# Kernel optimization log

Hardware: AMD Instinct MI355X
Metric: run time of the kernel (lower is better)

The kernel has to match this reference:

```python
import jax, jax.numpy as jnp
import numpy as np

EPS = 1e-5
C = 512


def conv1x1(x, w, b):
    # 1x1 conv == per-pixel linear: x [B,C,H,W], w [O,C], b [O]
    return jnp.einsum('bchw,oc->bohw', x, w) + b[None, :, None, None]


def mean_variance_norm(feat):
    # per (batch, channel) normalization over spatial dims, unbiased var + eps
    b, c, h, w = feat.shape
    flat = feat.reshape(b, c, h * w)
    mean = flat.mean(axis=2)[:, :, None, None]
    std = jnp.sqrt(jnp.var(flat, axis=2, ddof=1) + EPS)[:, :, None, None]
    return (feat - mean) / std


def setup_inputs() -> dict:
    key = jax.random.key(0)
    ks = jax.random.split(key, 10)
    sc = 1.0 / np.sqrt(C)
    inp = {
        'content': jax.random.normal(ks[0], (2, C, 64, 64), jnp.float32),
        'style': jax.random.normal(ks[1], (2, C, 64, 64), jnp.float32),
        'f_w': jax.random.normal(ks[2], (C, C), jnp.float32) * sc,
        'f_b': jnp.zeros((C,), jnp.float32),
        'g_w': jax.random.normal(ks[3], (C, C), jnp.float32) * sc,
        'g_b': jnp.zeros((C,), jnp.float32),
        'h_w': jax.random.normal(ks[4], (C, C), jnp.float32) * sc,
        'h_b': jnp.zeros((C,), jnp.float32),
        'out_w': jax.random.normal(ks[5], (C, C), jnp.float32) * sc,
        'out_b': jnp.zeros((C,), jnp.float32),
    }
    return inp


def reference(content, style, f_w, f_b, g_w, g_b, h_w, h_b, out_w, out_b):
    b, c, h, w = content.shape
    Fq = conv1x1(content, f_w, f_b).reshape(b, c, h * w).transpose(0, 2, 1)  # [b,Nc,C]
    Gk = conv1x1(style, g_w, g_b).reshape(b, c, -1)                           # [b,C,Ns]
    Hv = conv1x1(style, h_w, h_b).reshape(b, c, -1).transpose(0, 2, 1)        # [b,Ns,C]

    S = jax.nn.softmax(jnp.einsum('bnc,bcs->bns', Fq, Gk), axis=-1)           # [b,Nc,Ns]
    mean = jnp.einsum('bns,bsc->bnc', S, Hv)                                   # E[x]
    second = jnp.einsum('bns,bsc->bnc', S, Hv * Hv)                            # E[x^2]
    std = jnp.sqrt(jnp.maximum(second - mean * mean, 0.0))

    mean = mean.reshape(b, h, w, c).transpose(0, 3, 1, 2)
    std = std.reshape(b, h, w, c).transpose(0, 3, 1, 2)

    O = std * mean_variance_norm(content) + mean
    O = conv1x1(O, out_w, out_b)
    return O + content
```

## Files before the change

### kernel.cpp

```cpp
#include <hip/hip_runtime.h>
#include <math.h>

#define NS 4096
#define CH 512
#define EPSV 1e-5f

typedef __attribute__((ext_vector_type(8))) _Float16 f16x8;
typedef __attribute__((ext_vector_type(4))) float f32x4;
typedef unsigned short u16;

__device__ __forceinline__ u16 f2h(float x) {
    _Float16 h = (_Float16)x;
    return __builtin_bit_cast(unsigned short, h);
}
__device__ __forceinline__ float h2f(u16 b) {
    return (float)__builtin_bit_cast(_Float16, b);
}

__device__ __forceinline__ void gload16(const void* g, void* l) {
    __builtin_amdgcn_global_load_lds((const __attribute__((address_space(1))) unsigned*)g,
                                     (__attribute__((address_space(3))) unsigned*)l, 16, 0, 0);
}

struct ZTab {
    long aoff[6];
    long boff[6];
    long ooff[6];
    int  mode[6];
    int  np[6];
    const float* bias[6];
};

template<int NPZ>
__device__ __forceinline__ void kloop(
    const u16* __restrict__ pAhi, const u16* __restrict__ pAlo,
    const u16* __restrict__ pBhi, const u16* __restrict__ pBlo,
    u16* smem, int smemStride,
    int Mw, int Nw, int K, int m0, int n0,
    int wid, int lane, int lk, int lm, int wm, int wn,
    f32x4 (&acc)[4][4])
{
    auto stage = [&](int buf, int ks) {
        const int kp0 = ks << 2;
        #pragma unroll
        for (int i = 0; i < 2 * NPZ; ++i) {
            const int q = i * 4 + wid;
            const int b = q >> 3;
            const int p = (q & 7) >> 1;
            const int w = ((q & 1) << 6) + lane;
            const u16* src;
            if (b == 0)      src = pAhi + ((size_t)(kp0 + p) * Mw + m0 + w) * 8;
            else if (b == 1) src = pBhi + ((size_t)(kp0 + p) * Nw + n0 + w) * 8;
            else if (b == 2) src = pAlo + ((size_t)(kp0 + p) * Mw + m0 + w) * 8;
            else             src = pBlo + ((size_t)(kp0 + p) * Nw + n0 + w) * 8;
            gload16(src, &smem[(size_t)buf * smemStride + (size_t)(((b * 4 + p) * 128) + w) * 8]);
        }
    };

    const int nK = K >> 5;
    stage(0, 0);
    __syncthreads();
    int cur = 0;
    for (int ks = 0; ks < nK; ++ks) {
        if (ks + 1 < nK) stage(cur ^ 1, ks + 1);
        const u16* sm = smem + (size_t)cur * smemStride;
        f16x8 ah[4], bh[4], al[4], bl[4];
        #pragma unroll
        for (int f = 0; f < 4; ++f) {
            ah[f] = *(const f16x8*)&sm[((0 * 4 + lk) * 128 + wm * 64 + f * 16 + lm) * 8];
            bh[f] = *(const f16x8*)&sm[((1 * 4 + lk) * 128 + wn * 64 + f * 16 + lm) * 8];
            if (NPZ >= 3)
                al[f] = *(const f16x8*)&sm[((2 * 4 + lk) * 128 + wm * 64 + f * 16 + lm) * 8];
            if (NPZ == 4)
                bl[f] = *(const f16x8*)&sm[((3 * 4 + lk) * 128 + wn * 64 + f * 16 + lm) * 8];
        }
        #pragma unroll
        for (int i = 0; i < 4; ++i)
            #pragma unroll
            for (int j = 0; j < 4; ++j) {
                acc[i][j] = __builtin_amdgcn_mfma_f32_16x16x32_f16(ah[i], bh[j], acc[i][j], 0, 0, 0);
                if (NPZ >= 3)
                    acc[i][j] = __builtin_amdgcn_mfma_f32_16x16x32_f16(al[i], bh[j], acc[i][j], 0, 0, 0);
                if (NPZ == 4)
                    acc[i][j] = __builtin_amdgcn_mfma_f32_16x16x32_f16(ah[i], bl[j], acc[i][j], 0, 0, 0);
            }
        __syncthreads();
        cur ^= 1;
    }
}

template<int NP, bool RESID, bool COLST>
__global__ __launch_bounds__(256, (NP == 2 ? 4 : (NP == 3 ? 3 : 2))) void gemm_split(
    const u16* __restrict__ Ahi, const u16* __restrict__ Alo,
    const u16* __restrict__ Bhi, const u16* __restrict__ Blo,
    const float* __restrict__ resid,
    float* __restrict__ outF, u16* __restrict__ outH,
    float* __restrict__ pmg, float* __restrict__ psg,
    int Mw, int Nw, int K, ZTab tab)
{
    __shared__ u16 smem[2][NP * 4 * 128 * 8];
    const int t = threadIdx.x;
    const int lane = t & 63;
    const int wid = t >> 6;
    const int wm = wid >> 1, wn = wid & 1;
    const int lk = lane >> 4, lm = lane & 15;
    const int m0 = blockIdx.y * 128, n0 = blockIdx.x * 128;
    const int z = blockIdx.z;
    const int npz = tab.np[z];
    const u16* pAhi = Ahi + tab.aoff[z];
    const u16* pAlo = Alo + tab.aoff[z];
    const u16* pBhi = Bhi + tab.boff[z];
    const u16* pBlo = (NP == 4) ? (Blo + tab.boff[z]) : nullptr;

    f32x4 acc[4][4] = {};
    const int smemStride = NP * 4 * 128 * 8;

    if constexpr (NP == 2) {
        kloop<2>(pAhi, pAlo, pBhi, pBlo, &smem[0][0], smemStride,
                 Mw, Nw, K, m0, n0, wid, lane, lk, lm, wm, wn, acc);
    } else if constexpr (NP == 3) {
        if (npz == 2)
            kloop<2>(pAhi, pAlo, pBhi, pBlo, &smem[0][0], smemStride,
                     Mw, Nw, K, m0, n0, wid, lane, lk, lm, wm, wn, acc);
        else
            kloop<3>(pAhi, pAlo, pBhi, pBlo, &smem[0][0], smemStride,
                     Mw, Nw, K, m0, n0, wid, lane, lk, lm, wm, wn, acc);
    } else {
        kloop<4>(pAhi, pAlo, pBhi, pBlo, &smem[0][0], smemStride,
                 Mw, Nw, K, m0, n0, wid, lane, lk, lm, wm, wn, acc);
    }

    const float* bp = tab.bias[z];
    if (COLST) {
        float mxj[4];
        #pragma unroll
        for (int j = 0; j < 4; ++j) {
            float mx = -3.0e38f;
            #pragma unroll
            for (int i = 0; i < 4; ++i)
                #pragma unroll
                for (int r = 0; r < 4; ++r)
                    mx = fmaxf(mx, acc[i][j][r]);
            mx = fmaxf(mx, __shfl_xor(mx, 16));
            mx = fmaxf(mx, __shfl_xor(mx, 32));
            mxj[j] = mx;
            float sum = 0.f;
            #pragma unroll
            for (int i = 0; i < 4; ++i)
                #pragma unroll
                for (int r = 0; r < 4; ++r)
                    sum += __expf(acc[i][j][r] - mx);
            sum += __shfl_xor(sum, 16);
            sum += __shfl_xor(sum, 32);
            if (lk == 0) {
                const int n = n0 + wn * 64 + j * 16 + lm;
                const int grp = (m0 >> 6) + wm;
                pmg[((size_t)z * 64 + grp) * NS + n] = mx;
                psg[((size_t)z * 64 + grp) * NS + n] = sum;
            }
        }
        u16* ph = outH + tab.ooff[z];
        #pragma unroll
        for (int i = 0; i < 4; ++i) {
            const long rg = (long)((m0 + wm * 64) >> 3) + i * 2 + (lk >> 1);
            const int sub = (lk & 1) * 4;
            #pragma unroll
            for (int j = 0; j < 4; ++j) {
                const int n = n0 + wn * 64 + j * 16 + lm;
                const long idx = (rg * Nw + n) * 8 + sub;
                u16 h[4];
                #pragma unroll
                for (int r = 0; r < 4; ++r)
                    h[r] = f2h(acc[i][j][r] - mxj[j]);
                *(ushort4*)&ph[idx] = make_ushort4(h[0], h[1], h[2], h[3]);
            }
        }
    } else if (tab.mode[z] == 0) {
        float* pout = outF + tab.ooff[z];
        #pragma unroll
        for (int i = 0; i < 4; ++i) {
            #pragma unroll
            for (int r = 0; r < 4; ++r) {
                const int m = m0 + wm * 64 + i * 16 + lk * 4 + r;
                const float bv = bp ? bp[m] : 0.f;
                const size_t ro = (size_t)m * Nw + n0 + wn * 64 + lm;
                #pragma unroll
                for (int j = 0; j < 4; ++j) {
                    float v = acc[i][j][r] + bv;
                    if (RESID) v += resid[tab.ooff[z] + ro + j * 16];
                    pout[ro + j * 16] = v;
                }
            }
        }
    } else {
        u16* ph = outH + tab.ooff[z];
        #pragma unroll
        for (int i = 0; i < 4; ++i) {
            float bv[4];
            #pragma unroll
            for (int r = 0; r < 4; ++r) {
                const int m = m0 + wm * 64 + i * 16 + lk * 4 + r;
                bv[r] = bp ? bp[m] : 0.f;
            }
            const long rg = (long)((m0 + wm * 64) >> 3) + i * 2 + (lk >> 1);
            const int sub = (lk & 1) * 4;
            #pragma unroll
            for (int j = 0; j < 4; ++j) {
                const int n = n0 + wn * 64 + j * 16 + lm;
                const long idx = (rg * Nw + n) * 8 + sub;
                u16 h[4];
                #pragma unroll
                for (int r = 0; r < 4; ++r)
                    h[r] = f2h(acc[i][j][r] + bv[r]);
                *(ushort4*)&ph[idx] = make_ushort4(h[0], h[1], h[2], h[3]);
            }
        }
    }
}

__global__ __launch_bounds__(256) void packB_k(const float* __restrict__ X,
    u16* __restrict__ Hi, int Nw, long xB, long pB)
{
    const int n = blockIdx.x * 256 + threadIdx.x;
    const int p = blockIdx.y;
    const int z = blockIdx.z;
    const float* Xp = X + (size_t)z * xB + ((size_t)p * 8) * Nw + n;
    u16 hi[8];
    #pragma unroll
    for (int j = 0; j < 8; ++j)
        hi[j] = f2h(Xp[(size_t)j * Nw]);
    const size_t o = (size_t)z * pB + ((size_t)p * Nw + n) * 8;
    *(uint4*)&Hi[o] = *(const uint4*)hi;
}

__global__ __launch_bounds__(256) void pack_P(const u16* __restrict__ S16,
    const float* __restrict__ pm, const float* __restrict__ mxv,
    const float* __restrict__ invv, u16* __restrict__ Pp)
{
    const int n = blockIdx.x * 256 + threadIdx.x;
    const int rg = blockIdx.y;
    const int z = blockIdx.z;
    const long NSNS = (long)NS * NS;
    const int g = rg >> 3;
    const float shift = pm[((size_t)z * 64 + g) * NS + n] - mxv[(size_t)z * NS + n];
    const float inv = invv[(size_t)z * NS + n];
    const size_t idx = (size_t)z * NSNS + ((size_t)rg * NS + n) * 8;
    uint4 sv = *(const uint4*)&S16[idx];
    const u16* s = (const u16*)&sv;
    u16 p[8];
    #pragma unroll
    for (int j = 0; j < 8; ++j)
        p[j] = f2h(__expf(h2f(s[j]) + shift) * inv);
    *(uint4*)&Pp[idx] = *(const uint4*)p;
}

__global__ __launch_bounds__(256) void packA_T(const float* __restrict__ W,
    u16* __restrict__ Hi, u16* __restrict__ Lo, int Kdim)
{
    __shared__ float tile[64][65];
    const int t = threadIdx.x;
    const int k0 = blockIdx.x * 64, m0 = blockIdx.y * 64;
    const int kk = t & 63, mb = t >> 6;
    #pragma unroll
    for (int it = 0; it < 16; ++it) {
        int mm = mb + it * 4;
        tile[mm][kk] = W[(size_t)(m0 + mm) * Kdim + k0 + kk];
    }
    __syncthreads();
    #pragma unroll
    for (int cc = 0; cc < 2; ++cc) {
        int c = t + cc * 256;
        int kp = c >> 6, m = c & 63;
        u16 hi[8], lo[8];
        #pragma unroll
        for (int j = 0; j < 8; ++j) {
            float v = tile[m][kp * 8 + j];
            u16 h = f2h(v);
            hi[j] = h;
            lo[j] = f2h(v - h2f(h));
        }
        size_t o = ((size_t)(k0 / 8 + kp) * CH + m0 + m) * 8;
        *(uint4*)&Hi[o] = *(const uint4*)hi;
        *(uint4*)&Lo[o] = *(const uint4*)lo;
    }
}

__global__ __launch_bounds__(256) void pack_hvT(const float* __restrict__ Hv,
    u16* __restrict__ H1h, u16* __restrict__ H2h, u16* __restrict__ H2l)
{
    __shared__ float tile[64][65];
    const int t = threadIdx.x;
    const int s0 = blockIdx.x * 64, c0 = blockIdx.y * 64;
    const int z = blockIdx.z;
    const float* src = Hv + (size_t)z * CH * NS;
    const int ss = t & 63, cb = t >> 6;
    #pragma unroll
    for (int it = 0; it < 16; ++it) {
        int cc = cb + it * 4;
        tile[cc][ss] = src[(size_t)(c0 + cc) * NS + s0 + ss];
    }
    __syncthreads();
    const size_t zb = (size_t)z * NS * CH;
    #pragma unroll
    for (int cc2 = 0; cc2 < 2; ++cc2) {
        int c = t + cc2 * 256;
        int sp = c >> 6, cm = c & 63;
        u16 h1[8], h2[8], l2[8];
        #pragma unroll
        for (int j = 0; j < 8; ++j) {
            float v = tile[cm][sp * 8 + j];
            u16 a = f2h(v);
            h1[j] = a;
            float q = h2f(a);
            float q2 = q * q;
            u16 b = f2h(q2);
            h2[j] = b;
            l2[j] = f2h(q2 - h2f(b));
        }
        size_t o = zb + ((size_t)(s0 / 8 + sp) * CH + c0 + cm) * 8;
        *(uint4*)&H1h[o] = *(const uint4*)h1;
        *(uint4*)&H2h[o] = *(const uint4*)h2;
        *(uint4*)&H2l[o] = *(const uint4*)l2;
    }
}

__global__ __launch_bounds__(256) void colstats_comb64(const float* __restrict__ pm,
    const float* __restrict__ ps, float* __restrict__ mx, float* __restrict__ inv)
{
    const int n = blockIdx.x * 256 + threadIdx.x;
    const int z = blockIdx.y;
    float m = -3.0e38f, s = 0.f;
    #pragma unroll 8
    for (int g = 0; g < 64; ++g) {
        float gm = pm[((size_t)z * 64 + g) * NS + n], gs = ps[((size_t)z * 64 + g) * NS + n];
        float nm = fmaxf(m, gm);
        s = s * __expf(m - nm) + gs * __expf(gm - nm);
        m = nm;
    }
    mx[(size_t)z * NS + n] = m;
    inv[(size_t)z * NS + n] = 1.f / s;
}

__global__ __launch_bounds__(256) void content_stats(const float* __restrict__ content,
                                                     float* __restrict__ cmean,
                                                     float* __restrict__ cinv)
{
    const int bc = blockIdx.x;
    const float4* p = (const float4*)(content + (size_t)bc * NS);
    const int t = threadIdx.x;
    float s = 0.f, s2 = 0.f;
    #pragma unroll
    for (int j = 0; j < 4; ++j) {
        float4 v = p[t + j * 256];
        s  += (v.x + v.y) + (v.z + v.w);
        s2 += (v.x * v.x + v.y * v.y) + (v.z * v.z + v.w * v.w);
    }
    #pragma unroll
    for (int off = 32; off >= 1; off >>= 1) {
        s  += __shfl_xor(s, off);
        s2 += __shfl_xor(s2, off);
    }
    __shared__ float r1[4], r2[4];
    const int wid = t >> 6;
    if ((t & 63) == 0) { r1[wid] = s; r2[wid] = s2; }
    __syncthreads();
    if (t == 0) {
        s  = (r1[0] + r1[1]) + (r1[2] + r1[3]);
        s2 = (r2[0] + r2[1]) + (r2[2] + r2[3]);
        const float mean = s * (1.0f / 4096.f);
        const float var = (s2 - 4096.f * mean * mean) * (1.0f / 4095.f);
        cmean[bc] = mean;
        cinv[bc] = rsqrtf(fmaxf(var, 0.f) + EPSV);
    }
}

__global__ __launch_bounds__(256) void compute_O_pack(
    const float* __restrict__ Mean, const float* __restrict__ Sec,
    const float* __restrict__ content,
    const float* __restrict__ cmean, const float* __restrict__ cinv,
    u16* __restrict__ Oh)
{
    const int n  = blockIdx.x * 256 + threadIdx.x;
    const int cg = blockIdx.y;
    const int b  = blockIdx.z;
    const size_t KN = (size_t)CH * NS;
    u16 h[8];
    #pragma unroll
    for (int j = 0; j < 8; ++j) {
        const int c = cg * 8 + j;
        const size_t po = (size_t)b * KN + (size_t)c * NS + n;
        const float mn = Mean[po];
        const float sc = Sec[po];
        const float ct = content[po];
        const int bc = b * CH + c;
        const float o = sqrtf(fmaxf(sc - mn * mn, 0.f)) * ((ct - cmean[bc]) * cinv[bc]) + mn;
        h[j] = f2h(o);
    }
    const size_t off = (size_t)b * KN + ((size_t)cg * NS + n) * 8;
    *(uint4*)&Oh[off] = *(const uint4*)h;
}

extern "C" void kernel_launch(void* const* d_in, const int* in_sizes, int n_in,
                              void* d_out, int out_size, void* d_ws, size_t ws_size,
                              hipStream_t stream)
{
    const float* content = (const float*)d_in[0];
    const float* style   = (const float*)d_in[1];
    const float* f_w   = (const float*)d_in[2];
    const float* f_b   = (const float*)d_in[3];
    const float* g_w   = (const float*)d_in[4];
    const float* g_b   = (const float*)d_in[5];
    const float* h_w   = (const float*)d_in[6];
    const float* h_b   = (const float*)d_in[7];
    const float* out_w = (const float*)d_in[8];
    const float* out_b = (const float*)d_in[9];
    float* out = (float*)d_out;

    char* ws = (char*)d_ws;
    size_t off = 0;
    auto alloc = [&](size_t bytes) -> void* {
        void* p = ws + off;
        off = (off + bytes + 255) & ~(size_t)255;
        return p;
    };

    const size_t KN   = (size_t)CH * NS;
    const size_t CHCH = (size_t)CH * CH;
    const long   NSNS = (long)NS * NS;

    u16 *Wh[4], *Wl[4];
    for (int w = 0; w < 4; ++w) { Wh[w] = (u16*)alloc(CHCH * 2); Wl[w] = (u16*)alloc(CHCH * 2); }

    u16* R2 = (u16*)alloc(8 * KN * 2);
    u16* Xc_hi = R2;
    u16* Xs_hi = R2 + 2 * KN;
    u16* HvT_hi  = R2;
    u16* Hv2T_hi = R2 + 2 * KN;
    u16* Hv2T_lo = R2 + 4 * KN;

    u16* Fqp_hi = (u16*)alloc(2 * KN * 2);
    u16* Gkp_hi = (u16*)alloc(2 * KN * 2);
    u16* Op_hi  = Gkp_hi;

    u16* Pp = (u16*)alloc(2 * (size_t)NS * NS * 2);

    char* R5 = (char*)alloc(2 * (size_t)NS * NS * 2);
    float* Hv32 = (float*)(R5 + 4 * KN * 4);
    u16*   S16  = (u16*)R5;

    float* Mean32 = (float*)alloc(2 * KN * 4);
    float* Sec32  = (float*)alloc(2 * KN * 4);

    float* pm    = (float*)alloc(2 * 64 * NS * 4);
    float* ps    = (float*)alloc(2 * 64 * NS * 4);
    float* mxv   = (float*)alloc(2 * NS * 4);
    float* invv  = (float*)alloc(2 * NS * 4);
    float* cmean = (float*)alloc(1024 * 4);
    float* cinv  = (float*)alloc(1024 * 4);
    (void)ws_size; (void)in_sizes; (void)n_in; (void)out_size;

    packA_T<<<dim3(8, 8), 256, 0, stream>>>(f_w,   Wh[0], Wl[0], CH);
    packA_T<<<dim3(8, 8), 256, 0, stream>>>(g_w,   Wh[1], Wl[1], CH);
    packA_T<<<dim3(8, 8), 256, 0, stream>>>(h_w,   Wh[2], Wl[2], CH);
    packA_T<<<dim3(8, 8), 256, 0, stream>>>(out_w, Wh[3], Wl[3], CH);
    packB_k<<<dim3(16, 64, 2), 256, 0, stream>>>(content, Xc_hi, NS, (long)KN, (long)KN);
    packB_k<<<dim3(16, 64, 2), 256, 0, stream>>>(style,   Xs_hi, NS, (long)KN, (long)KN);
    content_stats<<<1024, 256, 0, stream>>>(content, cmean, cinv);

    {
        ZTab tb = {};
        const float* bs[3] = { f_b, g_b, h_b };
        for (int z = 0; z < 6; ++z) {
            const int w = z >> 1, b = z & 1;
            tb.aoff[z] = (long)(2 * w) * CHCH;
            tb.boff[z] = (w == 0 ? 0 : (long)(2 * KN)) + (long)b * KN;
            tb.mode[z] = (w < 2) ? 1 : 0;
            tb.np[z]   = 3;
            tb.ooff[z] = (w < 2) ? ((long)w * 2 * KN + (long)b * KN)
                                 : ((long)4 * KN + (long)b * KN);
            tb.bias[z] = bs[w];
        }
        gemm_split<3, false, false><<<dim3(32, 4, 6), 256, 0, stream>>>(
            Wh[0], Wh[0] + CHCH, Xc_hi, nullptr, nullptr,
            (float*)R5, Fqp_hi, nullptr, nullptr, CH, NS, CH, tb);
    }

    pack_hvT<<<dim3(64, 8, 2), 256, 0, stream>>>(Hv32, HvT_hi, Hv2T_hi, Hv2T_lo);

    {
        ZTab tq = {};
        for (int z = 0; z < 2; ++z) {
            tq.aoff[z] = (long)z * KN;
            tq.boff[z] = (long)z * KN;
            tq.ooff[z] = (long)z * NSNS;
            tq.np[z]   = 2;
        }
        gemm_split<2, false, true><<<dim3(32, 32, 2), 256, 0, stream>>>(
            Gkp_hi, nullptr, Fqp_hi, nullptr, nullptr,
            nullptr, S16, pm, ps, NS, NS, CH, tq);
    }
    colstats_comb64<<<dim3(16, 2), 256, 0, stream>>>(pm, ps, mxv, invv);
    pack_P<<<dim3(16, 512, 2), 256, 0, stream>>>(S16, pm, mxv, invv, Pp);

    {
        ZTab tp = {};
        for (int z = 0; z < 4; ++z) {
            const int sec = (z >> 1), b = z & 1;
            tp.aoff[z] = (long)sec * 2 * KN + (long)b * KN;
            tp.boff[z] = (long)b * NSNS;
            tp.ooff[z] = (long)sec * 2 * KN + (long)b * KN;
            tp.np[z]   = sec ? 3 : 2;
        }
        gemm_split<3, false, false><<<dim3(32, 4, 4), 256, 0, stream>>>(
            R2, R2 + 2 * KN, Pp, nullptr, nullptr,
            Mean32, nullptr, nullptr, nullptr, CH, NS, NS, tp);
    }

    compute_O_pack<<<dim3(16, 64, 2), 256, 0, stream>>>(
        Mean32, Sec32, content, cmean, cinv, Op_hi);

    {
        ZTab tf = {};
        for (int z = 0; z < 2; ++z) {
            tf.ooff[z] = (long)z * KN;
            tf.boff[z] = (long)z * KN;
            tf.np[z]   = 3;
            tf.bias[z] = out_b;
        }
        gemm_split<3, true, false><<<dim3(32, 4, 2), 256, 0, stream>>>(
            Wh[3], Wh[3] + CHCH, Op_hi, nullptr, content,
            out, nullptr, nullptr, nullptr, CH, NS, CH, tf);
    }
}
```

Baseline: 262.7 us.

## Fuse softmax exp into QK GEMM, apply per-group scale in PV GEMM, drop weight lo-split

The QK GEMM epilogue now combines the two warp-row max/sum partials in shared memory and writes exp(s - blockmax) in fp16 directly, halving the partial-stat groups. The separate pack_P pass over the full NSxNS matrix is removed. The PV GEMM instead accumulates each 128-row K group into a temporary and rescales it by a per-column factor from a small scale_c kernel. The hi/lo split of the weights for the 1x1 convs is also dropped (np 3 to 2), which cuts MFMA work but lowers precision of those projections.

```diff
diff --git a/kernel.cpp b/kernel.cpp
--- a/kernel.cpp
+++ b/kernel.cpp
@@ -26,18 +26,20 @@
     long aoff[6];
     long boff[6];
     long ooff[6];
+    long coff[6];
     int  mode[6];
     int  np[6];
     const float* bias[6];
 };
 
-template<int NPZ>
+template<int NPZ, bool GS>
 __device__ __forceinline__ void kloop(
     const u16* __restrict__ pAhi, const u16* __restrict__ pAlo,
-    const u16* __restrict__ pBhi, const u16* __restrict__ pBlo,
+    const u16* __restrict__ pBhi,
     u16* smem, int smemStride,
     int Mw, int Nw, int K, int m0, int n0,
     int wid, int lane, int lk, int lm, int wm, int wn,
+    const float* __restrict__ cbase, const int* nidx,
     f32x4 (&acc)[4][4])
 {
     auto stage = [&](int buf, int ks) {
@@ -51,51 +53,85 @@
             const u16* src;
             if (b == 0)      src = pAhi + ((size_t)(kp0 + p) * Mw + m0 + w) * 8;
             else if (b == 1) src = pBhi + ((size_t)(kp0 + p) * Nw + n0 + w) * 8;
-            else if (b == 2) src = pAlo + ((size_t)(kp0 + p) * Mw + m0 + w) * 8;
-            else             src = pBlo + ((size_t)(kp0 + p) * Nw + n0 + w) * 8;
+            else             src = pAlo + ((size_t)(kp0 + p) * Mw + m0 + w) * 8;
             gload16(src, &smem[(size_t)buf * smemStride + (size_t)(((b * 4 + p) * 128) + w) * 8]);
+        }
+    };
+    auto frags = [&](int buf, f16x8 (&ah)[4], f16x8 (&bh)[4], f16x8 (&al)[4]) {
+        const u16* sm = smem + (size_t)buf * smemStride;
+        #pragma unroll
+        for (int f = 0; f < 4; ++f) {
+            ah[f] = *(const f16x8*)&sm[((0 * 4 + lk) * 128 + wm * 64 + f * 16 + lm) * 8];
+            bh[f] = *(const f16x8*)&sm[((1 * 4 + lk) * 128 + wn * 64 + f * 16 + lm) * 8];
+            if (NPZ == 3)
+                al[f] = *(const f16x8*)&sm[((2 * 4 + lk) * 128 + wm * 64 + f * 16 + lm) * 8];
         }
     };
 
     const int nK = K >> 5;
     stage(0, 0);
     __syncthreads();
-    int cur = 0;
-    for (int ks = 0; ks < nK; ++ks) {
-        if (ks + 1 < nK) stage(cur ^ 1, ks + 1);
-        const u16* sm = smem + (size_t)cur * smemStride;
-        f16x8 ah[4], bh[4], al[4], bl[4];
-        #pragma unroll
-        for (int f = 0; f < 4; ++f) {
-            ah[f] = *(const f16x8*)&sm[((0 * 4 + lk) * 128 + wm * 64 + f * 16 + lm) * 8];
-            bh[f] = *(const f16x8*)&sm[((1 * 4 + lk) * 128 + wn * 64 + f * 16 + lm) * 8];
-            if (NPZ >= 3)
-                al[f] = *(const f16x8*)&sm[((2 * 4 + lk) * 128 + wm * 64 + f * 16 + lm) * 8];
-            if (NPZ == 4)
-                bl[f] = *(const f16x8*)&sm[((3 * 4 + lk) * 128 + wn * 64 + f * 16 + lm) * 8];
-        }
-        #pragma unroll
-        for (int i = 0; i < 4; ++i)
-            #pragma unroll
-            for (int j = 0; j < 4; ++j) {
-                acc[i][j] = __builtin_amdgcn_mfma_f32_16x16x32_f16(ah[i], bh[j], acc[i][j], 0, 0, 0);
-                if (NPZ >= 3)
-                    acc[i][j] = __builtin_amdgcn_mfma_f32_16x16x32_f16(al[i], bh[j], acc[i][j], 0, 0, 0);
-                if (NPZ == 4)
-                    acc[i][j] = __builtin_amdgcn_mfma_f32_16x16x32_f16(ah[i], bl[j], acc[i][j], 0, 0, 0);
-            }
-        __syncthreads();
-        cur ^= 1;
-    }
-}
-
-template<int NP, bool RESID, bool COLST>
-__global__ __launch_bounds__(256, (NP == 2 ? 4 : (NP == 3 ? 3 : 2))) void gemm_split(
+    if constexpr (GS) {
+        const f32x4 zf = {0.f, 0.f, 0.f, 0.f};
+        const int nG = nK >> 2;
+        for (int g = 0; g < nG; ++g) {
+            float cg[4];
+            #pragma unroll
+            for (int j = 0; j < 4; ++j)
+                cg[j] = cbase[(size_t)g * NS + nidx[j]];
+            f32x4 part[4][4];
+            #pragma unroll
+            for (int kk = 0; kk < 4; ++kk) {
+                const int ks = g * 4 + kk;
+                if (ks + 1 < nK) stage((kk & 1) ^ 1, ks + 1);
+                f16x8 ah[4], bh[4], al[4];
+                frags(kk & 1, ah, bh, al);
+                #pragma unroll
+                for (int i = 0; i < 4; ++i)
+                    #pragma unroll
+                    for (int j = 0; j < 4; ++j) {
+                        part[i][j] = __builtin_amdgcn_mfma_f32_16x16x32_f16(
+                            ah[i], bh[j], (kk == 0 ? zf : part[i][j]), 0, 0, 0);
+                        if (NPZ == 3)
+                            part[i][j] = __builtin_amdgcn_mfma_f32_16x16x32_f16(
+                                al[i], bh[j], part[i][j], 0, 0, 0);
+                    }
+                __syncthreads();
+            }
+            #pragma unroll
+            for (int i = 0; i < 4; ++i)
+                #pragma unroll
+                for (int j = 0; j < 4; ++j)
+                    acc[i][j] += part[i][j] * cg[j];
+        }
+    } else {
+        int cur = 0;
+        for (int ks = 0; ks < nK; ++ks) {
+            if (ks + 1 < nK) stage(cur ^ 1, ks + 1);
+            f16x8 ah[4], bh[4], al[4];
+            frags(cur, ah, bh, al);
+            #pragma unroll
+            for (int i = 0; i < 4; ++i)
+                #pragma unroll
+                for (int j = 0; j < 4; ++j) {
+                    acc[i][j] = __builtin_amdgcn_mfma_f32_16x16x32_f16(ah[i], bh[j], acc[i][j], 0, 0, 0);
+                    if (NPZ == 3)
+                        acc[i][j] = __builtin_amdgcn_mfma_f32_16x16x32_f16(al[i], bh[j], acc[i][j], 0, 0, 0);
+                }
+            __syncthreads();
+            cur ^= 1;
+        }
+    }
+}
+
+template<int NP, bool RESID, bool COLST, bool GS>
+__global__ __launch_bounds__(256, (NP == 2 ? 4 : 3)) void gemm_split(
     const u16* __restrict__ Ahi, const u16* __restrict__ Alo,
-    const u16* __restrict__ Bhi, const u16* __restrict__ Blo,
+    const u16* __restrict__ Bhi,
     const float* __restrict__ resid,
     float* __restrict__ outF, u16* __restrict__ outH,
     float* __restrict__ pmg, float* __restrict__ psg,
+    const float* __restrict__ cb,
     int Mw, int Nw, int K, ZTab tab)
 {
     __shared__ u16 smem[2][NP * 4 * 128 * 8];
@@ -110,29 +146,31 @@
     const u16* pAhi = Ahi + tab.aoff[z];
     const u16* pAlo = Alo + tab.aoff[z];
     const u16* pBhi = Bhi + tab.boff[z];
-    const u16* pBlo = (NP == 4) ? (Blo + tab.boff[z]) : nullptr;
+    const float* cbase = GS ? (cb + tab.coff[z]) : nullptr;
+    int nidx[4];
+    #pragma unroll
+    for (int j = 0; j < 4; ++j) nidx[j] = n0 + wn * 64 + j * 16 + lm;
 
     f32x4 acc[4][4] = {};
     const int smemStride = NP * 4 * 128 * 8;
 
     if constexpr (NP == 2) {
-        kloop<2>(pAhi, pAlo, pBhi, pBlo, &smem[0][0], smemStride,
-                 Mw, Nw, K, m0, n0, wid, lane, lk, lm, wm, wn, acc);
-    } else if constexpr (NP == 3) {
+        kloop<2, GS>(pAhi, pAlo, pBhi, &smem[0][0], smemStride,
+                     Mw, Nw, K, m0, n0, wid, lane, lk, lm, wm, wn, cbase, nidx, acc);
+    } else {
         if (npz == 2)
-            kloop<2>(pAhi, pAlo, pBhi, pBlo, &smem[0][0], smemStride,
-                     Mw, Nw, K, m0, n0, wid, lane, lk, lm, wm, wn, acc);
+            kloop<2, GS>(pAhi, pAlo, pBhi, &smem[0][0], smemStride,
+                         Mw, Nw, K, m0, n0, wid, lane, lk, lm, wm, wn, cbase, nidx, acc);
         else
-            kloop<3>(pAhi, pAlo, pBhi, pBlo, &smem[0][0], smemStride,
-                     Mw, Nw, K, m0, n0, wid, lane, lk, lm, wm, wn, acc);
-    } else {
-        kloop<4>(pAhi, pAlo, pBhi, pBlo, &smem[0][0], smemStride,
-                 Mw, Nw, K, m0, n0, wid, lane, lk, lm, wm, wn, acc);
+            kloop<3, GS>(pAhi, pAlo, pBhi, &smem[0][0], smemStride,
+                         Mw, Nw, K, m0, n0, wid, lane, lk, lm, wm, wn, cbase, nidx, acc);
     }
 
     const float* bp = tab.bias[z];
     if (COLST) {
-        float mxj[4];
+        float* smx = (float*)&smem[0][0];
+        float* ssm = smx + 256;
+        float mxw[4], smw[4];
         #pragma unroll
         for (int j = 0; j < 4; ++j) {
             float mx = -3.0e38f;
@@ -143,7 +181,6 @@
                     mx = fmaxf(mx, acc[i][j][r]);
             mx = fmaxf(mx, __shfl_xor(mx, 16));
             mx = fmaxf(mx, __shfl_xor(mx, 32));
-            mxj[j] = mx;
             float sum = 0.f;
             #pragma unroll
             for (int i = 0; i < 4; ++i)
@@ -152,11 +189,27 @@
                     sum += __expf(acc[i][j][r] - mx);
             sum += __shfl_xor(sum, 16);
             sum += __shfl_xor(sum, 32);
+            mxw[j] = mx; smw[j] = sum;
             if (lk == 0) {
-                const int n = n0 + wn * 64 + j * 16 + lm;
-                const int grp = (m0 >> 6) + wm;
-                pmg[((size_t)z * 64 + grp) * NS + n] = mx;
-                psg[((size_t)z * 64 + grp) * NS + n] = sum;
+                const int nloc = wn * 64 + j * 16 + lm;
+                smx[wm * 128 + nloc] = mx;
+                ssm[wm * 128 + nloc] = sum;
+            }
+        }
+        __syncthreads();
+        float mxc[4];
+        #pragma unroll
+        for (int j = 0; j < 4; ++j) {
+            const int nloc = wn * 64 + j * 16 + lm;
+            const float m0v = smx[nloc], m1v = smx[128 + nloc];
+            const float mc = fmaxf(m0v, m1v);
+            mxc[j] = mc;
+            if (wm == 0 && lk == 0) {
+                const float sc = ssm[nloc] * __expf(m0v - mc) + ssm[128 + nloc] * __expf(m1v - mc);
+                const int n = n0 + nloc;
+                const size_t gi = ((size_t)z * 32 + (m0 >> 7)) * NS + n;
+                pmg[gi] = mc;
+                psg[gi] = sc;
             }
         }
         u16* ph = outH + tab.ooff[z];
@@ -171,7 +224,7 @@
                 u16 h[4];
                 #pragma unroll
                 for (int r = 0; r < 4; ++r)
-                    h[r] = f2h(acc[i][j][r] - mxj[j]);
+                    h[r] = f2h(__expf(acc[i][j][r] - mxc[j]));
                 *(ushort4*)&ph[idx] = make_ushort4(h[0], h[1], h[2], h[3]);
             }
         }
@@ -233,29 +286,8 @@
     *(uint4*)&Hi[o] = *(const uint4*)hi;
 }
 
-__global__ __launch_bounds__(256) void pack_P(const u16* __restrict__ S16,
-    const float* __restrict__ pm, const float* __restrict__ mxv,
-    const float* __restrict__ invv, u16* __restrict__ Pp)
-{
-    const int n = blockIdx.x * 256 + threadIdx.x;
-    const int rg = blockIdx.y;
-    const int z = blockIdx.z;
-    const long NSNS = (long)NS * NS;
-    const int g = rg >> 3;
-    const float shift = pm[((size_t)z * 64 + g) * NS + n] - mxv[(size_t)z * NS + n];
-    const float inv = invv[(size_t)z * NS + n];
-    const size_t idx = (size_t)z * NSNS + ((size_t)rg * NS + n) * 8;
-    uint4 sv = *(const uint4*)&S16[idx];
-    const u16* s = (const u16*)&sv;
-    u16 p[8];
-    #pragma unroll
-    for (int j = 0; j < 8; ++j)
-        p[j] = f2h(__expf(h2f(s[j]) + shift) * inv);
-    *(uint4*)&Pp[idx] = *(const uint4*)p;
-}
-
 __global__ __launch_bounds__(256) void packA_T(const float* __restrict__ W,
-    u16* __restrict__ Hi, u16* __restrict__ Lo, int Kdim)
+    u16* __restrict__ Hi, int Kdim)
 {
     __shared__ float tile[64][65];
     const int t = threadIdx.x;
@@ -271,17 +303,12 @@
     for (int cc = 0; cc < 2; ++cc) {
         int c = t + cc * 256;
         int kp = c >> 6, m = c & 63;
-        u16 hi[8], lo[8];
-        #pragma unroll
-        for (int j = 0; j < 8; ++j) {
-            float v = tile[m][kp * 8 + j];
-            u16 h = f2h(v);
-            hi[j] = h;
-            lo[j] = f2h(v - h2f(h));
-        }
+        u16 hi[8];
+        #pragma unroll
+        for (int j = 0; j < 8; ++j)
+            hi[j] = f2h(tile[m][kp * 8 + j]);
         size_t o = ((size_t)(k0 / 8 + kp) * CH + m0 + m) * 8;
         *(uint4*)&Hi[o] = *(const uint4*)hi;
-        *(uint4*)&Lo[o] = *(const uint4*)lo;
     }
 }
 
@@ -324,21 +351,32 @@
     }
 }
 
-__global__ __launch_bounds__(256) void colstats_comb64(const float* __restrict__ pm,
+__global__ __launch_bounds__(256) void colstats_comb32(const float* __restrict__ pm,
     const float* __restrict__ ps, float* __restrict__ mx, float* __restrict__ inv)
 {
     const int n = blockIdx.x * 256 + threadIdx.x;
     const int z = blockIdx.y;
     float m = -3.0e38f, s = 0.f;
     #pragma unroll 8
-    for (int g = 0; g < 64; ++g) {
-        float gm = pm[((size_t)z * 64 + g) * NS + n], gs = ps[((size_t)z * 64 + g) * NS + n];
+    for (int g = 0; g < 32; ++g) {
+        float gm = pm[((size_t)z * 32 + g) * NS + n], gs = ps[((size_t)z * 32 + g) * NS + n];
         float nm = fmaxf(m, gm);
         s = s * __expf(m - nm) + gs * __expf(gm - nm);
         m = nm;
     }
     mx[(size_t)z * NS + n] = m;
     inv[(size_t)z * NS + n] = 1.f / s;
+}
+
+__global__ __launch_bounds__(256) void scale_c(const float* __restrict__ pm,
+    const float* __restrict__ mxv, const float* __restrict__ invv,
+    float* __restrict__ c)
+{
+    const int n = blockIdx.x * 256 + threadIdx.x;
+    const int g = blockIdx.y;
+    const int z = blockIdx.z;
+    const size_t gi = ((size_t)z * 32 + g) * NS + n;
+    c[gi] = __expf(pm[gi] - mxv[(size_t)z * NS + n]) * invv[(size_t)z * NS + n];
 }
 
 __global__ __launch_bounds__(256) void content_stats(const float* __restrict__ content,
@@ -428,10 +466,10 @@
     const size_t CHCH = (size_t)CH * CH;
     const long   NSNS = (long)NS * NS;
 
-    u16 *Wh[4], *Wl[4];
-    for (int w = 0; w < 4; ++w) { Wh[w] = (u16*)alloc(CHCH * 2); Wl[w] = (u16*)alloc(CHCH * 2); }
-
-    u16* R2 = (u16*)alloc(8 * KN * 2);
+    u16* Wh0 = (u16*)alloc(4 * CHCH * 2);
+    u16* Whv[4] = { Wh0, Wh0 + CHCH, Wh0 + 2 * CHCH, Wh0 + 3 * CHCH };
+
+    u16* R2 = (u16*)alloc(6 * KN * 2);
     u16* Xc_hi = R2;
     u16* Xs_hi = R2 + 2 * KN;
     u16* HvT_hi  = R2;
@@ -442,27 +480,26 @@
     u16* Gkp_hi = (u16*)alloc(2 * KN * 2);
     u16* Op_hi  = Gkp_hi;
 
-    u16* Pp = (u16*)alloc(2 * (size_t)NS * NS * 2);
-
     char* R5 = (char*)alloc(2 * (size_t)NS * NS * 2);
     float* Hv32 = (float*)(R5 + 4 * KN * 4);
-    u16*   S16  = (u16*)R5;
+    u16*   E16  = (u16*)R5;
 
     float* Mean32 = (float*)alloc(2 * KN * 4);
     float* Sec32  = (float*)alloc(2 * KN * 4);
 
-    float* pm    = (float*)alloc(2 * 64 * NS * 4);
-    float* ps    = (float*)alloc(2 * 64 * NS * 4);
+    float* pm    = (float*)alloc(2 * 32 * NS * 4);
+    float* ps    = (float*)alloc(2 * 32 * NS * 4);
     float* mxv   = (float*)alloc(2 * NS * 4);
     float* invv  = (float*)alloc(2 * NS * 4);
+    float* ctab  = (float*)alloc(2 * 32 * NS * 4);
     float* cmean = (float*)alloc(1024 * 4);
     float* cinv  = (float*)alloc(1024 * 4);
     (void)ws_size; (void)in_sizes; (void)n_in; (void)out_size;
 
-    packA_T<<<dim3(8, 8), 256, 0, stream>>>(f_w,   Wh[0], Wl[0], CH);
-    packA_T<<<dim3(8, 8), 256, 0, stream>>>(g_w,   Wh[1], Wl[1], CH);
-    packA_T<<<dim3(8, 8), 256, 0, stream>>>(h_w,   Wh[2], Wl[2], CH);
-    packA_T<<<dim3(8, 8), 256, 0, stream>>>(out_w, Wh[3], Wl[3], CH);
+    packA_T<<<dim3(8, 8), 256, 0, stream>>>(f_w,   Whv[0], CH);
+    packA_T<<<dim3(8, 8), 256, 0, stream>>>(g_w,   Whv[1], CH);
+    packA_T<<<dim3(8, 8), 256, 0, stream>>>(h_w,   Whv[2], CH);
+    packA_T<<<dim3(8, 8), 256, 0, stream>>>(out_w, Whv[3], CH);
     packB_k<<<dim3(16, 64, 2), 256, 0, stream>>>(content, Xc_hi, NS, (long)KN, (long)KN);
     packB_k<<<dim3(16, 64, 2), 256, 0, stream>>>(style,   Xs_hi, NS, (long)KN, (long)KN);
     content_stats<<<1024, 256, 0, stream>>>(content, cmean, cinv);
@@ -472,17 +509,17 @@
         const float* bs[3] = { f_b, g_b, h_b };
         for (int z = 0; z < 6; ++z) {
             const int w = z >> 1, b = z & 1;
-            tb.aoff[z] = (long)(2 * w) * CHCH;
+            tb.aoff[z] = (long)w * CHCH;
             tb.boff[z] = (w == 0 ? 0 : (long)(2 * KN)) + (long)b * KN;
             tb.mode[z] = (w < 2) ? 1 : 0;
-            tb.np[z]   = 3;
+            tb.np[z]   = 2;
             tb.ooff[z] = (w < 2) ? ((long)w * 2 * KN + (long)b * KN)
                                  : ((long)4 * KN + (long)b * KN);
             tb.bias[z] = bs[w];
         }
-        gemm_split<3, false, false><<<dim3(32, 4, 6), 256, 0, stream>>>(
-            Wh[0], Wh[0] + CHCH, Xc_hi, nullptr, nullptr,
-            (float*)R5, Fqp_hi, nullptr, nullptr, CH, NS, CH, tb);
+        gemm_split<2, false, false, false><<<dim3(32, 4, 6), 256, 0, stream>>>(
+            Wh0, nullptr, Xc_hi, nullptr,
+            (float*)R5, Fqp_hi, nullptr, nullptr, nullptr, CH, NS, CH, tb);
     }
 
     pack_hvT<<<dim3(64, 8, 2), 256, 0, stream>>>(Hv32, HvT_hi, Hv2T_hi, Hv2T_lo);
@@ -495,12 +532,12 @@
             tq.ooff[z] = (long)z * NSNS;
             tq.np[z]   = 2;
         }
-        gemm_split<2, false, true><<<dim3(32, 32, 2), 256, 0, stream>>>(
-            Gkp_hi, nullptr, Fqp_hi, nullptr, nullptr,
-            nullptr, S16, pm, ps, NS, NS, CH, tq);
-    }
-    colstats_comb64<<<dim3(16, 2), 256, 0, stream>>>(pm, ps, mxv, invv);
-    pack_P<<<dim3(16, 512, 2), 256, 0, stream>>>(S16, pm, mxv, invv, Pp);
+        gemm_split<2, false, true, false><<<dim3(32, 32, 2), 256, 0, stream>>>(
+            Gkp_hi, nullptr, Fqp_hi, nullptr,
+            nullptr, E16, pm, ps, nullptr, NS, NS, CH, tq);
+    }
+    colstats_comb32<<<dim3(16, 2), 256, 0, stream>>>(pm, ps, mxv, invv);
+    scale_c<<<dim3(16, 32, 2), 256, 0, stream>>>(pm, mxv, invv, ctab);
 
     {
         ZTab tp = {};
@@ -509,11 +546,12 @@
             tp.aoff[z] = (long)sec * 2 * KN + (long)b * KN;
             tp.boff[z] = (long)b * NSNS;
             tp.ooff[z] = (long)sec * 2 * KN + (long)b * KN;
+            tp.coff[z] = (long)b * 32 * NS;
             tp.np[z]   = sec ? 3 : 2;
         }
-        gemm_split<3, false, false><<<dim3(32, 4, 4), 256, 0, stream>>>(
-            R2, R2 + 2 * KN, Pp, nullptr, nullptr,
-            Mean32, nullptr, nullptr, nullptr, CH, NS, NS, tp);
+        gemm_split<3, false, false, true><<<dim3(32, 4, 4), 256, 0, stream>>>(
+            R2, R2 + 2 * KN, E16, nullptr,
+            Mean32, nullptr, nullptr, nullptr, ctab, CH, NS, NS, tp);
     }
 
     compute_O_pack<<<dim3(16, 64, 2), 256, 0, stream>>>(
@@ -524,11 +562,11 @@
         for (int z = 0; z < 2; ++z) {
             tf.ooff[z] = (long)z * KN;
             tf.boff[z] = (long)z * KN;
-            tf.np[z]   = 3;
+            tf.np[z]   = 2;
             tf.bias[z] = out_b;
         }
-        gemm_split<3, true, false><<<dim3(32, 4, 2), 256, 0, stream>>>(
-            Wh[3], Wh[3] + CHCH, Op_hi, nullptr, content,
-            out, nullptr, nullptr, nullptr, CH, NS, CH, tf);
-    }
-}
+        gemm_split<2, true, false, false><<<dim3(32, 4, 2), 256, 0, stream>>>(
+            Whv[3], nullptr, Op_hi, content,
+            out, nullptr, nullptr, nullptr, nullptr, CH, NS, CH, tf);
+    }
+}
```

After: 526.7 us. 2x slower.
